# Kernel optimization log

Hardware: AMD Instinct MI355X
Metric: run time of the kernel (lower is better)

## Reference

```python
import jax, jax.numpy as jnp
import numpy as np

D = 768      # feature_dim
HD = 768     # hidden_dim
NH = 4       # num_heads
B, T1, T2 = 4, 128, 128
LN_EPS = 1e-5

def setup_inputs() -> dict:
    key = jax.random.key(0)
    ks = jax.random.split(key, 12)
    s = 0.02
    return {
        'speech_features': jax.random.normal(ks[0], (B, T1, D), jnp.float32),
        'phoneme_features': jax.random.normal(ks[1], (B, T2, D), jnp.float32),
        # per-head attention MLP: Linear(2D->HD), ReLU, Linear(HD->1); stacked over heads
        'W1': jax.random.normal(ks[2], (NH, 2 * D, HD), jnp.float32) * s,
        'b1': jnp.zeros((NH, HD), jnp.float32),
        'w2': jax.random.normal(ks[3], (NH, HD), jnp.float32) * s,
        'b2': jnp.zeros((NH,), jnp.float32),
        # fusion: Linear(2D->2HD), ReLU, Linear(2HD->D), LayerNorm(D)
        'Wf1': jax.random.normal(ks[4], (2 * D, 2 * HD), jnp.float32) * s,
        'bf1': jnp.zeros((2 * HD,), jnp.float32),
        'Wf2': jax.random.normal(ks[5], (2 * HD, D), jnp.float32) * s,
        'bf2': jnp.zeros((D,), jnp.float32),
        'ln_g': jnp.ones((D,), jnp.float32),
        'ln_b': jnp.zeros((D,), jnp.float32),
    }

def reference(speech_features, phoneme_features, W1, b1, w2, b2, Wf1, bf1, Wf2, bf2, ln_g, ln_b):
    d = speech_features.shape[-1]
    # Decompose Linear(cat([speech_t, phoneme])) = speech@W1[:d] + phoneme@W1[d:] + b1
    Wx, Wy = W1[:, :d, :], W1[:, d:, :]
    sx = jnp.einsum('btd,ndh->nbth', speech_features, Wx)   # [NH,B,T1,HD]
    py = jnp.einsum('bsd,ndh->nbsh', phoneme_features, Wy)  # [NH,B,T2,HD]
    hidden = jax.nn.relu(sx[:, :, :, None, :] + py[:, :, None, :, :]
                         + b1[:, None, None, None, :])      # [NH,B,T1,T2,HD]
    scores = jnp.einsum('nbtsh,nh->nbts', hidden, w2) + b2[:, None, None, None]
    attn = jax.nn.softmax(scores, axis=-1).mean(axis=0)     # [B,T1,T2]
    context = jnp.einsum('bts,bsd->btd', attn, phoneme_features)  # [B,T1,D]
    fused = jnp.concatenate([speech_features, context], axis=-1)  # [B,T1,2D]
    # dropout is identity in eval mode
    h = jax.nn.relu(fused @ Wf1 + bf1)
    out = h @ Wf2 + bf2
    mu = out.mean(axis=-1, keepdims=True)
    var = ((out - mu) ** 2).mean(axis=-1, keepdims=True)
    out = (out - mu) * jax.lax.rsqrt(var + LN_EPS) * ln_g + ln_b
    return out.mean(axis=1)  # [B,D]
```

## Files before the change

kernel.cpp:

```cpp
#include <hip/hip_runtime.h>
#include <cstddef>


#define D_  768
#define HD_ 768
#define NH_ 4
#define B_  4
#define T1_ 128
#define T2_ 128
#define M_  (B_*T1_)
#define LN_EPS_ 1e-5f

typedef unsigned short u16;
typedef unsigned int u32;
typedef _Float16 f16;
typedef _Float16 f16x2 __attribute__((ext_vector_type(2)));
typedef __bf16 bf16x8 __attribute__((ext_vector_type(8)));
typedef float f32x4 __attribute__((ext_vector_type(4)));

__device__ __forceinline__ u16 f2bf(float f) {
    union { float f; unsigned int u; } v; v.f = f;
    unsigned int u = v.u + (0x7FFFu + ((v.u >> 16) & 1u));
    return (u16)(u >> 16);
}
__device__ __forceinline__ u16 f16bits(f16 h) {
    return __builtin_bit_cast(unsigned short, h);
}
__device__ __forceinline__ f16x2 bcast2(u32 u) {
    return __builtin_bit_cast(f16x2, u);
}
__device__ __forceinline__ u32 splat2(u16 h) { return (u32)h * 0x10001u; }

template<bool RELU, int MODE>
__device__ __forceinline__ void gemm_mfma_body(
    const u16* __restrict__ A, int lda,
    const u16* __restrict__ Bt, int ldb,
    const float* __restrict__ bias,
    void* __restrict__ C, int ldc, int K, int m0, int n0)
{
    __shared__ __align__(16) u16 As[64][40];
    __shared__ __align__(16) u16 Bs[64][40];
    __shared__ u16 Ts[MODE == 3 ? 64 : 1][MODE == 3 ? 68 : 1];

    const int tid = threadIdx.x;
    const int row = tid >> 2;
    const int kq  = (tid & 3) << 3;
    const int lane = tid & 63;
    const int w  = tid >> 6;
    const int wr = (w >> 1) << 5;
    const int wc = (w & 1) << 5;
    const int l16 = lane & 15;
    const int lk8 = (lane >> 4) << 3;
    const int r4  = (lane >> 4) << 2;

    const u16* aptr = A + (size_t)(m0 + row) * lda + kq;
    const u16* bptr = Bt + (size_t)(n0 + row) * ldb + kq;

    f32x4 acc00 = {0.f,0.f,0.f,0.f}, acc01 = {0.f,0.f,0.f,0.f};
    f32x4 acc10 = {0.f,0.f,0.f,0.f}, acc11 = {0.f,0.f,0.f,0.f};

    uint4 a_nxt = *(const uint4*)aptr;
    uint4 b_nxt = *(const uint4*)bptr;

    for (int k0 = 0; k0 < K; k0 += 32) {
        __syncthreads();
        *(uint4*)&As[row][kq] = a_nxt;
        *(uint4*)&Bs[row][kq] = b_nxt;
        if (k0 + 32 < K) {
            a_nxt = *(const uint4*)(aptr + k0 + 32);
            b_nxt = *(const uint4*)(bptr + k0 + 32);
        }
        __syncthreads();
        bf16x8 af0 = *(const bf16x8*)&As[wr + l16][lk8];
        bf16x8 af1 = *(const bf16x8*)&As[wr + 16 + l16][lk8];
        bf16x8 bf0 = *(const bf16x8*)&Bs[wc + l16][lk8];
        bf16x8 bf1 = *(const bf16x8*)&Bs[wc + 16 + l16][lk8];
        acc00 = __builtin_amdgcn_mfma_f32_16x16x32_bf16(af0, bf0, acc00, 0, 0, 0);
        acc01 = __builtin_amdgcn_mfma_f32_16x16x32_bf16(af0, bf1, acc01, 0, 0, 0);
        acc10 = __builtin_amdgcn_mfma_f32_16x16x32_bf16(af1, bf0, acc10, 0, 0, 0);
        acc11 = __builtin_amdgcn_mfma_f32_16x16x32_bf16(af1, bf1, acc11, 0, 0, 0);
    }

#define EPI_FRAG(ACC, MF, NF)                                                  \
    {                                                                          \
        const int gcol = n0 + wc + (NF)*16 + l16;                              \
        const float bv = bias ? bias[gcol] : 0.f;                              \
        float v_[4];                                                           \
        _Pragma("unroll")                                                      \
        for (int r = 0; r < 4; r++) {                                          \
            float v = ACC[r] + bv;                                             \
            if (RELU) v = fmaxf(v, 0.f);                                       \
            v_[r] = v;                                                         \
        }                                                                      \
        const int lr0 = wr + (MF)*16 + r4;                                     \
        if (MODE == 3) {                                                       \
            const int lc = wc + (NF)*16 + l16;                                 \
            _Pragma("unroll")                                                  \
            for (int r = 0; r < 4; r++) Ts[lc][lr0 + r] = f16bits((f16)v_[r]); \
        } else {                                                               \
            _Pragma("unroll")                                                  \
            for (int r = 0; r < 4; r++) {                                      \
                const size_t off = (size_t)(m0 + lr0 + r) * ldc + gcol;        \
                if (MODE == 0) ((float*)C)[off] = v_[r];                       \
                else if (MODE == 1) ((u16*)C)[off] = f2bf(v_[r]);              \
                else ((u16*)C)[off] = f16bits((f16)v_[r]);                     \
            }                                                                  \
        }                                                                      \
    }
    EPI_FRAG(acc00, 0, 0) EPI_FRAG(acc01, 0, 1)
    EPI_FRAG(acc10, 1, 0) EPI_FRAG(acc11, 1, 1)
#undef EPI_FRAG

    if (MODE == 3) {
        __syncthreads();
        u16* cb = (u16*)C + (size_t)(m0 >> 7) * (768 * 128) + (m0 & 127);
#pragma unroll
        for (int u = 0; u < 4; u++) {
            const int i = tid + u * 256;
            const int hl = i >> 4;
            const int s4 = (i & 15) << 2;
            ushort4 o;
            o.x = Ts[hl][s4 + 0]; o.y = Ts[hl][s4 + 1];
            o.z = Ts[hl][s4 + 2]; o.w = Ts[hl][s4 + 3];
            *(ushort4*)(cb + (size_t)(n0 + hl) * 128 + s4) = o;
        }
    }
}

__global__ __launch_bounds__(256) void prep_kernel(
    const float* __restrict__ speech, const float* __restrict__ phon,
    const float* __restrict__ W1, const float* __restrict__ Wf1,
    const float* __restrict__ Wf2,
    u16* __restrict__ spb, u16* __restrict__ phb,
    u16* __restrict__ w1t, u16* __restrict__ wf1t, u16* __restrict__ wf2t)
{
    const int tid = threadIdx.x;
    int bid = blockIdx.x;
    if (bid < 768) {
        const bool isp = bid < 384;
        const float* in = isp ? speech : phon;
        u16* outb = isp ? spb : phb;
        const int i = ((isp ? bid : bid - 384) * 256 + tid) * 4;
        float4 v = *(const float4*)(in + i);
        ushort4 o;
        o.x = f2bf(v.x); o.y = f2bf(v.y); o.z = f2bf(v.z); o.w = f2bf(v.w);
        *(ushort4*)(outb + i) = o;
        return;
    }
    bid -= 768;
    const float* in; u16* outp; int tx, ty;
    if (bid < 4608) {
        const int z = bid / 1152, r = bid % 1152;
        tx = r % 24; ty = r / 24;
        in = W1 + (size_t)z * 1536 * 768; outp = w1t + (size_t)z * 768 * 1536;
    } else if (bid < 6912) {
        const int r = bid - 4608;
        tx = r % 48; ty = r / 48;
        in = Wf1; outp = wf1t;
    } else {
        const int r = bid - 6912;
        tx = r % 24; ty = r / 24;
        in = Wf2; outp = wf2t;
    }
    const int C = (bid >= 4608 && bid < 6912) ? 1536 : 768;
    const int c0 = tx * 32, r0 = ty * 32;
    __shared__ float tile[32][33];
    const int tr = tid >> 3, tc = (tid & 7) << 2;
    float4 v = *(const float4*)(in + (size_t)(r0 + tr) * C + c0 + tc);
    tile[tr][tc] = v.x; tile[tr][tc + 1] = v.y;
    tile[tr][tc + 2] = v.z; tile[tr][tc + 3] = v.w;
    __syncthreads();
    ushort4 o;
    o.x = f2bf(tile[tc + 0][tr]); o.y = f2bf(tile[tc + 1][tr]);
    o.z = f2bf(tile[tc + 2][tr]); o.w = f2bf(tile[tc + 3][tr]);
    *(ushort4*)(outp + (size_t)(c0 + tr) * 1536 + r0 + tc) = o;
}

__global__ __launch_bounds__(256) void gemm_sxpy_kernel(
    const u16* __restrict__ sp, const u16* __restrict__ ph,
    const u16* __restrict__ w1t, const float* __restrict__ b1,
    u16* __restrict__ sxf, u16* __restrict__ pyt)
{
    const int z = blockIdx.z;
    const int n = z & 3;
    const bool ispy = z >= 4;
    const u16* Bt = w1t + (size_t)n * 768 * 1536 + (ispy ? 768 : 0);
    if (!ispy) {
        gemm_mfma_body<false, 2>(sp, 768, Bt, 1536, b1 + n * HD_,
                                 sxf + (size_t)n * M_ * HD_, HD_, 768,
                                 blockIdx.y * 64, blockIdx.x * 64);
    } else {
        gemm_mfma_body<false, 3>(ph, 768, Bt, 1536, nullptr,
                                 pyt + (size_t)n * 4 * 768 * 128, 0, 768,
                                 blockIdx.y * 64, blockIdx.x * 64);
    }
}

template<bool RELU, int MODE>
__global__ __launch_bounds__(256) void gemm_mfma_kernel(
    const u16* __restrict__ A, int lda,
    const u16* __restrict__ Bt, int ldb,
    const float* __restrict__ bias,
    void* __restrict__ C, int ldc, int K)
{
    gemm_mfma_body<RELU, MODE>(A, lda, Bt, ldb, bias, C, ldc, K,
                               blockIdx.y * 64, blockIdx.x * 64);
}

__global__ __launch_bounds__(256) void scores_softmax_kernel(
    const u16* __restrict__ sxf,
    const u16* __restrict__ pyt,
    const float* __restrict__ w2,
    float* __restrict__ probs)
{
    const int bid = blockIdx.x;
    const int n = bid >> 7, b = (bid >> 5) & 3, t0 = (bid & 31) * 4;
    const int tid = threadIdx.x, lane = tid & 63, w = tid >> 6;

    __shared__ __align__(16) f16x2 sxs[4][768];
    __shared__ __align__(16) f16x2 w2s[768];

#pragma unroll
    for (int q = 0; q < 3; q++) {
        const int u = tid + q * 256;
        const int r = u / 192;
        const int h4 = (u % 192) * 4;
        ushort4 v = *(const ushort4*)(sxf + ((size_t)(n * 512 + b * 128 + t0 + r)) * 768 + h4);
        sxs[r][h4 + 0] = bcast2(splat2(v.x));
        sxs[r][h4 + 1] = bcast2(splat2(v.y));
        sxs[r][h4 + 2] = bcast2(splat2(v.z));
        sxs[r][h4 + 3] = bcast2(splat2(v.w));
    }
#pragma unroll
    for (int q = 0; q < 3; q++) {
        const int i = tid + q * 256;
        w2s[i] = bcast2(splat2(f16bits((f16)w2[n * 768 + i])));
    }
    __syncthreads();

    const f16x2* pypanel = (const f16x2*)(pyt + ((size_t)((n << 2) | b)) * 768 * 128) + lane;
    const f16x2 z2 = {(f16)0, (f16)0};

    float acc0 = 0.f, acc1 = 0.f;

    f16x2 b0[16], b1[16];
#pragma unroll
    for (int j = 0; j < 16; j++) b0[j] = pypanel[(size_t)j * 64];
#pragma unroll
    for (int j = 0; j < 16; j++) b1[j] = pypanel[(size_t)(16 + j) * 64];

    for (int hc = 0; hc < 768; hc += 32) {
        f16x2 a4[4] = {z2, z2, z2, z2};
#pragma unroll
        for (int j = 0; j < 16; j++) {
            f16x2 r_ = __builtin_elementwise_max(sxs[w][hc + j] + b0[j], z2);
            a4[j & 3] = __builtin_elementwise_fma(r_, w2s[hc + j], a4[j & 3]);
        }
        if (hc + 32 < 768) {
#pragma unroll
            for (int j = 0; j < 16; j++) b0[j] = pypanel[(size_t)(hc + 32 + j) * 64];
        }
#pragma unroll
        for (int j = 0; j < 16; j++) {
            f16x2 r_ = __builtin_elementwise_max(sxs[w][hc + 16 + j] + b1[j], z2);
            a4[j & 3] = __builtin_elementwise_fma(r_, w2s[hc + 16 + j], a4[j & 3]);
        }
        if (hc + 48 < 768) {
#pragma unroll
            for (int j = 0; j < 16; j++) b1[j] = pypanel[(size_t)(hc + 48 + j) * 64];
        }
#pragma unroll
        for (int k = 0; k < 4; k++) {
            acc0 += (float)a4[k].x;
            acc1 += (float)a4[k].y;
        }
    }

    float mx = fmaxf(acc0, acc1);
#pragma unroll
    for (int off = 32; off; off >>= 1) mx = fmaxf(mx, __shfl_xor(mx, off, 64));
    const float e0 = expf(acc0 - mx), e1 = expf(acc1 - mx);
    float sm = e0 + e1;
#pragma unroll
    for (int off = 32; off; off >>= 1) sm += __shfl_xor(sm, off, 64);
    const float inv = 0.25f / sm;
    float2 pr; pr.x = e0 * inv; pr.y = e1 * inv;
    *(float2*)&probs[((size_t)(n * 512 + b * 128 + t0 + w)) * 128 + 2 * lane] = pr;
}

__global__ __launch_bounds__(256) void context_fused_kernel(
    const float* __restrict__ probs, const float* __restrict__ phon,
    const float* __restrict__ speech, u16* __restrict__ fused)
{
    const int m = blockIdx.x;
    const int b = m >> 7;
    const int tid = threadIdx.x;
    __shared__ float attn[T2_];
    if (tid < T2_) {
        float a = 0.f;
#pragma unroll
        for (int n = 0; n < NH_; n++)
            a += probs[(size_t)(n * M_ + m) * T2_ + tid];
        attn[tid] = a;
    }
    __syncthreads();
    const float* ph = phon + (size_t)b * T2_ * D_;
#pragma unroll
    for (int j = 0; j < 3; j++) {
        const int d = tid + 256 * j;
        float acc = 0.f;
#pragma unroll 8
        for (int s = 0; s < T2_; s++)
            acc = fmaf(attn[s], ph[(size_t)s * D_ + d], acc);
        fused[(size_t)m * (2 * D_) + d] = f2bf(speech[(size_t)m * D_ + d]);
        fused[(size_t)m * (2 * D_) + D_ + d] = f2bf(acc);
    }
}

__global__ __launch_bounds__(256) void ln_fused_kernel(
    const float* __restrict__ x, const float* __restrict__ g,
    const float* __restrict__ lb, float* __restrict__ out)
{
    const int b = blockIdx.x, tid = threadIdx.x, lane = tid & 63, w = tid >> 6;
    __shared__ float rs[T1_];
    __shared__ float Sred[4];

    float prsum = 0.f;
    for (int i = 0; i < 32; i++) {
        const int row = w * 32 + i;
        const float4* x4 = (const float4*)(x + ((size_t)(b * T1_ + row)) * D_);
        float s = 0.f, ss = 0.f;
#pragma unroll
        for (int j = 0; j < 3; j++) {
            float4 v = x4[j * 64 + lane];
            s += v.x + v.y + v.z + v.w;
            ss += v.x * v.x + v.y * v.y + v.z * v.z + v.w * v.w;
        }
#pragma unroll
        for (int off = 32; off; off >>= 1) {
            s += __shfl_xor(s, off, 64);
            ss += __shfl_xor(ss, off, 64);
        }
        if (lane == 0) {
            const float mu = s * (1.f / D_);
            const float var = ss * (1.f / D_) - mu * mu;
            const float r = rsqrtf(var + LN_EPS_);
            rs[row] = r;
            prsum += mu * r;
        }
    }
    if (lane == 0) Sred[w] = prsum;
    __syncthreads();
    const float S = Sred[0] + Sred[1] + Sred[2] + Sred[3];
    const float* xb = x + (size_t)b * T1_ * D_;
#pragma unroll
    for (int j = 0; j < 3; j++) {
        const int d = tid + 256 * j;
        float acc = 0.f;
#pragma unroll 8
        for (int t = 0; t < T1_; t++)
            acc = fmaf(xb[(size_t)t * D_ + d], rs[t], acc);
        out[b * D_ + d] = g[d] * (acc - S) * (1.f / T1_) + lb[d];
    }
}

extern "C" void kernel_launch(void* const* d_in, const int* in_sizes, int n_in,
                              void* d_out, int out_size, void* d_ws, size_t ws_size,
                              hipStream_t stream)
{
    const float* speech = (const float*)d_in[0];
    const float* phon   = (const float*)d_in[1];
    const float* W1     = (const float*)d_in[2];
    const float* b1     = (const float*)d_in[3];
    const float* w2     = (const float*)d_in[4];
    const float* Wf1    = (const float*)d_in[6];
    const float* bf1    = (const float*)d_in[7];
    const float* Wf2    = (const float*)d_in[8];
    const float* bf2    = (const float*)d_in[9];
    const float* ln_g   = (const float*)d_in[10];
    const float* ln_b   = (const float*)d_in[11];
    float* out = (float*)d_out;

    char* w = (char*)d_ws;
    auto alloc = [&](size_t bytes) { char* p = w; w += (bytes + 1023) & ~(size_t)1023; return p; };
    u16* sp_bf  = (u16*)alloc((size_t)M_ * D_ * 2);
    u16* ph_bf  = (u16*)alloc((size_t)M_ * D_ * 2);
    u16* w1t    = (u16*)alloc((size_t)NH_ * 768 * 1536 * 2);
    u16* wf1t   = (u16*)alloc((size_t)1536 * 1536 * 2);
    u16* wf2t   = (u16*)alloc((size_t)768 * 1536 * 2);
    u16* sxf    = (u16*)alloc((size_t)NH_ * M_ * HD_ * 2);
    u16* pyt    = (u16*)alloc((size_t)NH_ * B_ * 768 * 128 * 2);
    float* probs  = (float*)alloc((size_t)NH_ * M_ * T2_ * 4);
    u16* fusedb = (u16*)alloc((size_t)M_ * 2 * D_ * 2);
    u16* hbuf   = (u16*)alloc((size_t)M_ * 2 * HD_ * 2);
    float* outpre = (float*)alloc((size_t)M_ * D_ * 4);

    hipLaunchKernelGGL(prep_kernel, dim3(8832), dim3(256), 0, stream,
                       speech, phon, W1, Wf1, Wf2, sp_bf, ph_bf, w1t, wf1t, wf2t);
    hipLaunchKernelGGL(gemm_sxpy_kernel, dim3(HD_ / 64, M_ / 64, 8), dim3(256), 0, stream,
                       sp_bf, ph_bf, w1t, b1, sxf, pyt);
    hipLaunchKernelGGL(scores_softmax_kernel, dim3(512), dim3(256), 0, stream,
                       sxf, pyt, w2, probs);
    hipLaunchKernelGGL(context_fused_kernel, dim3(M_), dim3(256), 0, stream,
                       probs, phon, speech, fusedb);
    hipLaunchKernelGGL((gemm_mfma_kernel<true, 1>), dim3(2 * HD_ / 64, M_ / 64), dim3(256), 0, stream,
                       fusedb, 2 * D_, wf1t, 1536, bf1, hbuf, 2 * HD_, 2 * D_);
    hipLaunchKernelGGL((gemm_mfma_kernel<false, 0>), dim3(D_ / 64, M_ / 64), dim3(256), 0, stream,
                       hbuf, 2 * HD_, wf2t, 1536, bf2, outpre, D_, 2 * HD_);
    hipLaunchKernelGGL(ln_fused_kernel, dim3(B_), dim3(256), 0, stream,
                       outpre, ln_g, ln_b, out);
}
```

Measured before the change: 134.8 us.

## Fuse scores with context, convert activations in GEMM loads, split LN blocks

Drops the separate activation-to-bf16 conversion pass. The sx/py GEMM now reads fp32 speech and phoneme data and packs it to bf16 while loading. The scores/softmax kernel now handles all four heads of one query row, one wave per head, and sums their probabilities in shared memory before computing the context row directly, which removes the probs buffer and one launch. The final LayerNorm-mean kernel is split across 12 blocks instead of 4 to expose more parallelism, at the cost of each block recomputing the row statistics.

New measurement: 127.8 us. 5.2% less time.

```diff
diff --git a/kernel.cpp b/kernel.cpp
--- a/kernel.cpp
+++ b/kernel.cpp
@@ -23,6 +23,9 @@
     unsigned int u = v.u + (0x7FFFu + ((v.u >> 16) & 1u));
     return (u16)(u >> 16);
 }
+__device__ __forceinline__ u32 pack_bf2(float lo, float hi) {
+    return (u32)f2bf(lo) | ((u32)f2bf(hi) << 16);
+}
 __device__ __forceinline__ u16 f16bits(f16 h) {
     return __builtin_bit_cast(unsigned short, h);
 }
@@ -31,9 +34,9 @@
 }
 __device__ __forceinline__ u32 splat2(u16 h) { return (u32)h * 0x10001u; }
 
-template<bool RELU, int MODE>
+template<bool RELU, int MODE, bool AF32>
 __device__ __forceinline__ void gemm_mfma_body(
-    const u16* __restrict__ A, int lda,
+    const void* __restrict__ Av, int lda,
     const u16* __restrict__ Bt, int ldb,
     const float* __restrict__ bias,
     void* __restrict__ C, int ldc, int K, int m0, int n0)
@@ -53,13 +56,26 @@
     const int lk8 = (lane >> 4) << 3;
     const int r4  = (lane >> 4) << 2;
 
-    const u16* aptr = A + (size_t)(m0 + row) * lda + kq;
-    const u16* bptr = Bt + (size_t)(n0 + row) * ldb + kq;
+    const u16*   aptr16 = (const u16*)Av + (size_t)(m0 + row) * lda + kq;
+    const float* aptrf  = (const float*)Av + (size_t)(m0 + row) * lda + kq;
+    const u16*   bptr   = Bt + (size_t)(n0 + row) * ldb + kq;
 
     f32x4 acc00 = {0.f,0.f,0.f,0.f}, acc01 = {0.f,0.f,0.f,0.f};
     f32x4 acc10 = {0.f,0.f,0.f,0.f}, acc11 = {0.f,0.f,0.f,0.f};
 
-    uint4 a_nxt = *(const uint4*)aptr;
+    auto loadA = [&](int k0) -> uint4 {
+        if (AF32) {
+            float4 ax = *(const float4*)(aptrf + k0);
+            float4 ay = *(const float4*)(aptrf + k0 + 4);
+            uint4 r;
+            r.x = pack_bf2(ax.x, ax.y); r.y = pack_bf2(ax.z, ax.w);
+            r.z = pack_bf2(ay.x, ay.y); r.w = pack_bf2(ay.z, ay.w);
+            return r;
+        }
+        return *(const uint4*)(aptr16 + k0);
+    };
+
+    uint4 a_nxt = loadA(0);
     uint4 b_nxt = *(const uint4*)bptr;
 
     for (int k0 = 0; k0 < K; k0 += 32) {
@@ -67,7 +83,7 @@
         *(uint4*)&As[row][kq] = a_nxt;
         *(uint4*)&Bs[row][kq] = b_nxt;
         if (k0 + 32 < K) {
-            a_nxt = *(const uint4*)(aptr + k0 + 32);
+            a_nxt = loadA(k0 + 32);
             b_nxt = *(const uint4*)(bptr + k0 + 32);
         }
         __syncthreads();
@@ -128,26 +144,12 @@
 }
 
 __global__ __launch_bounds__(256) void prep_kernel(
-    const float* __restrict__ speech, const float* __restrict__ phon,
     const float* __restrict__ W1, const float* __restrict__ Wf1,
     const float* __restrict__ Wf2,
-    u16* __restrict__ spb, u16* __restrict__ phb,
     u16* __restrict__ w1t, u16* __restrict__ wf1t, u16* __restrict__ wf2t)
 {
     const int tid = threadIdx.x;
     int bid = blockIdx.x;
-    if (bid < 768) {
-        const bool isp = bid < 384;
-        const float* in = isp ? speech : phon;
-        u16* outb = isp ? spb : phb;
-        const int i = ((isp ? bid : bid - 384) * 256 + tid) * 4;
-        float4 v = *(const float4*)(in + i);
-        ushort4 o;
-        o.x = f2bf(v.x); o.y = f2bf(v.y); o.z = f2bf(v.z); o.w = f2bf(v.w);
-        *(ushort4*)(outb + i) = o;
-        return;
-    }
-    bid -= 768;
     const float* in; u16* outp; int tx, ty;
     if (bid < 4608) {
         const int z = bid / 1152, r = bid % 1152;
@@ -177,7 +179,7 @@
 }
 
 __global__ __launch_bounds__(256) void gemm_sxpy_kernel(
-    const u16* __restrict__ sp, const u16* __restrict__ ph,
+    const float* __restrict__ sp, const float* __restrict__ ph,
     const u16* __restrict__ w1t, const float* __restrict__ b1,
     u16* __restrict__ sxf, u16* __restrict__ pyt)
 {
@@ -186,13 +188,13 @@
     const bool ispy = z >= 4;
     const u16* Bt = w1t + (size_t)n * 768 * 1536 + (ispy ? 768 : 0);
     if (!ispy) {
-        gemm_mfma_body<false, 2>(sp, 768, Bt, 1536, b1 + n * HD_,
-                                 sxf + (size_t)n * M_ * HD_, HD_, 768,
-                                 blockIdx.y * 64, blockIdx.x * 64);
+        gemm_mfma_body<false, 2, true>(sp, 768, Bt, 1536, b1 + n * HD_,
+                                       sxf + (size_t)n * M_ * HD_, HD_, 768,
+                                       blockIdx.y * 64, blockIdx.x * 64);
     } else {
-        gemm_mfma_body<false, 3>(ph, 768, Bt, 1536, nullptr,
-                                 pyt + (size_t)n * 4 * 768 * 128, 0, 768,
-                                 blockIdx.y * 64, blockIdx.x * 64);
+        gemm_mfma_body<false, 3, true>(ph, 768, Bt, 1536, nullptr,
+                                       pyt + (size_t)n * 4 * 768 * 128, 0, 768,
+                                       blockIdx.y * 64, blockIdx.x * 64);
     }
 }
 
@@ -203,42 +205,45 @@
     const float* __restrict__ bias,
     void* __restrict__ C, int ldc, int K)
 {
-    gemm_mfma_body<RELU, MODE>(A, lda, Bt, ldb, bias, C, ldc, K,
-                               blockIdx.y * 64, blockIdx.x * 64);
-}
-
-__global__ __launch_bounds__(256) void scores_softmax_kernel(
+    gemm_mfma_body<RELU, MODE, false>(A, lda, Bt, ldb, bias, C, ldc, K,
+                                      blockIdx.y * 64, blockIdx.x * 64);
+}
+
+__global__ __launch_bounds__(256) void scores_ctx_kernel(
     const u16* __restrict__ sxf,
     const u16* __restrict__ pyt,
     const float* __restrict__ w2,
-    float* __restrict__ probs)
+    const float* __restrict__ phon,
+    const float* __restrict__ speech,
+    u16* __restrict__ fused)
 {
     const int bid = blockIdx.x;
-    const int n = bid >> 7, b = (bid >> 5) & 3, t0 = (bid & 31) * 4;
+    const int b = bid >> 7, t = bid & 127;
+    const int m = b * 128 + t;
     const int tid = threadIdx.x, lane = tid & 63, w = tid >> 6;
 
     __shared__ __align__(16) f16x2 sxs[4][768];
-    __shared__ __align__(16) f16x2 w2s[768];
+    __shared__ __align__(16) f16x2 w2s[4][768];
+    __shared__ float attn4[4][128];
+    __shared__ float attn[128];
 
 #pragma unroll
     for (int q = 0; q < 3; q++) {
-        const int u = tid + q * 256;
-        const int r = u / 192;
-        const int h4 = (u % 192) * 4;
-        ushort4 v = *(const ushort4*)(sxf + ((size_t)(n * 512 + b * 128 + t0 + r)) * 768 + h4);
-        sxs[r][h4 + 0] = bcast2(splat2(v.x));
-        sxs[r][h4 + 1] = bcast2(splat2(v.y));
-        sxs[r][h4 + 2] = bcast2(splat2(v.z));
-        sxs[r][h4 + 3] = bcast2(splat2(v.w));
-    }
-#pragma unroll
-    for (int q = 0; q < 3; q++) {
-        const int i = tid + q * 256;
-        w2s[i] = bcast2(splat2(f16bits((f16)w2[n * 768 + i])));
-    }
-    __syncthreads();
-
-    const f16x2* pypanel = (const f16x2*)(pyt + ((size_t)((n << 2) | b)) * 768 * 128) + lane;
+        const int u = lane + 64 * q;
+        const int h4 = u * 4;
+        ushort4 v = *(const ushort4*)(sxf + ((size_t)(w * 512 + m)) * 768 + h4);
+        sxs[w][h4 + 0] = bcast2(splat2(v.x));
+        sxs[w][h4 + 1] = bcast2(splat2(v.y));
+        sxs[w][h4 + 2] = bcast2(splat2(v.z));
+        sxs[w][h4 + 3] = bcast2(splat2(v.w));
+        float4 wv = *(const float4*)(w2 + w * 768 + h4);
+        w2s[w][h4 + 0] = bcast2(splat2(f16bits((f16)wv.x)));
+        w2s[w][h4 + 1] = bcast2(splat2(f16bits((f16)wv.y)));
+        w2s[w][h4 + 2] = bcast2(splat2(f16bits((f16)wv.z)));
+        w2s[w][h4 + 3] = bcast2(splat2(f16bits((f16)wv.w)));
+    }
+
+    const f16x2* pypanel = (const f16x2*)(pyt + ((size_t)((w << 2) | b)) * 768 * 128) + lane;
     const f16x2 z2 = {(f16)0, (f16)0};
 
     float acc0 = 0.f, acc1 = 0.f;
@@ -254,7 +259,7 @@
 #pragma unroll
         for (int j = 0; j < 16; j++) {
             f16x2 r_ = __builtin_elementwise_max(sxs[w][hc + j] + b0[j], z2);
-            a4[j & 3] = __builtin_elementwise_fma(r_, w2s[hc + j], a4[j & 3]);
+            a4[j & 3] = __builtin_elementwise_fma(r_, w2s[w][hc + j], a4[j & 3]);
         }
         if (hc + 32 < 768) {
 #pragma unroll
@@ -263,7 +268,7 @@
 #pragma unroll
         for (int j = 0; j < 16; j++) {
             f16x2 r_ = __builtin_elementwise_max(sxs[w][hc + 16 + j] + b1[j], z2);
-            a4[j & 3] = __builtin_elementwise_fma(r_, w2s[hc + 16 + j], a4[j & 3]);
+            a4[j & 3] = __builtin_elementwise_fma(r_, w2s[w][hc + 16 + j], a4[j & 3]);
         }
         if (hc + 48 < 768) {
 #pragma unroll
@@ -285,35 +290,23 @@
     for (int off = 32; off; off >>= 1) sm += __shfl_xor(sm, off, 64);
     const float inv = 0.25f / sm;
     float2 pr; pr.x = e0 * inv; pr.y = e1 * inv;
-    *(float2*)&probs[((size_t)(n * 512 + b * 128 + t0 + w)) * 128 + 2 * lane] = pr;
-}
-
-__global__ __launch_bounds__(256) void context_fused_kernel(
-    const float* __restrict__ probs, const float* __restrict__ phon,
-    const float* __restrict__ speech, u16* __restrict__ fused)
-{
-    const int m = blockIdx.x;
-    const int b = m >> 7;
-    const int tid = threadIdx.x;
-    __shared__ float attn[T2_];
-    if (tid < T2_) {
-        float a = 0.f;
-#pragma unroll
-        for (int n = 0; n < NH_; n++)
-            a += probs[(size_t)(n * M_ + m) * T2_ + tid];
-        attn[tid] = a;
-    }
+    *(float2*)&attn4[w][2 * lane] = pr;
     __syncthreads();
-    const float* ph = phon + (size_t)b * T2_ * D_;
+
+    if (tid < 128)
+        attn[tid] = attn4[0][tid] + attn4[1][tid] + attn4[2][tid] + attn4[3][tid];
+    __syncthreads();
+
+    const float* ph = phon + (size_t)b * 128 * 768;
 #pragma unroll
     for (int j = 0; j < 3; j++) {
         const int d = tid + 256 * j;
         float acc = 0.f;
 #pragma unroll 8
-        for (int s = 0; s < T2_; s++)
-            acc = fmaf(attn[s], ph[(size_t)s * D_ + d], acc);
-        fused[(size_t)m * (2 * D_) + d] = f2bf(speech[(size_t)m * D_ + d]);
-        fused[(size_t)m * (2 * D_) + D_ + d] = f2bf(acc);
+        for (int s = 0; s < 128; s++)
+            acc = fmaf(attn[s], ph[(size_t)s * 768 + d], acc);
+        fused[(size_t)m * 1536 + d] = f2bf(speech[(size_t)m * 768 + d]);
+        fused[(size_t)m * 1536 + 768 + d] = f2bf(acc);
     }
 }
 
@@ -321,7 +314,8 @@
     const float* __restrict__ x, const float* __restrict__ g,
     const float* __restrict__ lb, float* __restrict__ out)
 {
-    const int b = blockIdx.x, tid = threadIdx.x, lane = tid & 63, w = tid >> 6;
+    const int b = blockIdx.x / 3, c = blockIdx.x % 3;
+    const int tid = threadIdx.x, lane = tid & 63, w = tid >> 6;
     __shared__ float rs[T1_];
     __shared__ float Sred[4];
 
@@ -353,15 +347,12 @@
     __syncthreads();
     const float S = Sred[0] + Sred[1] + Sred[2] + Sred[3];
     const float* xb = x + (size_t)b * T1_ * D_;
-#pragma unroll
-    for (int j = 0; j < 3; j++) {
-        const int d = tid + 256 * j;
-        float acc = 0.f;
+    const int d = c * 256 + tid;
+    float acc = 0.f;
 #pragma unroll 8
-        for (int t = 0; t < T1_; t++)
-            acc = fmaf(xb[(size_t)t * D_ + d], rs[t], acc);
-        out[b * D_ + d] = g[d] * (acc - S) * (1.f / T1_) + lb[d];
-    }
+    for (int t = 0; t < T1_; t++)
+        acc = fmaf(xb[(size_t)t * D_ + d], rs[t], acc);
+    out[b * D_ + d] = g[d] * (acc - S) * (1.f / T1_) + lb[d];
 }
 
 extern "C" void kernel_launch(void* const* d_in, const int* in_sizes, int n_in,
@@ -383,30 +374,25 @@
 
     char* w = (char*)d_ws;
     auto alloc = [&](size_t bytes) { char* p = w; w += (bytes + 1023) & ~(size_t)1023; return p; };
-    u16* sp_bf  = (u16*)alloc((size_t)M_ * D_ * 2);
-    u16* ph_bf  = (u16*)alloc((size_t)M_ * D_ * 2);
     u16* w1t    = (u16*)alloc((size_t)NH_ * 768 * 1536 * 2);
     u16* wf1t   = (u16*)alloc((size_t)1536 * 1536 * 2);
     u16* wf2t   = (u16*)alloc((size_t)768 * 1536 * 2);
     u16* sxf    = (u16*)alloc((size_t)NH_ * M_ * HD_ * 2);
     u16* pyt    = (u16*)alloc((size_t)NH_ * B_ * 768 * 128 * 2);
-    float* probs  = (float*)alloc((size_t)NH_ * M_ * T2_ * 4);
     u16* fusedb = (u16*)alloc((size_t)M_ * 2 * D_ * 2);
     u16* hbuf   = (u16*)alloc((size_t)M_ * 2 * HD_ * 2);
     float* outpre = (float*)alloc((size_t)M_ * D_ * 4);
 
-    hipLaunchKernelGGL(prep_kernel, dim3(8832), dim3(256), 0, stream,
-                       speech, phon, W1, Wf1, Wf2, sp_bf, ph_bf, w1t, wf1t, wf2t);
+    hipLaunchKernelGGL(prep_kernel, dim3(8064), dim3(256), 0, stream,
+                       W1, Wf1, Wf2, w1t, wf1t, wf2t);
     hipLaunchKernelGGL(gemm_sxpy_kernel, dim3(HD_ / 64, M_ / 64, 8), dim3(256), 0, stream,
-                       sp_bf, ph_bf, w1t, b1, sxf, pyt);
-    hipLaunchKernelGGL(scores_softmax_kernel, dim3(512), dim3(256), 0, stream,
-                       sxf, pyt, w2, probs);
-    hipLaunchKernelGGL(context_fused_kernel, dim3(M_), dim3(256), 0, stream,
-                       probs, phon, speech, fusedb);
+                       speech, phon, w1t, b1, sxf, pyt);
+    hipLaunchKernelGGL(scores_ctx_kernel, dim3(512), dim3(256), 0, stream,
+                       sxf, pyt, w2, phon, speech, fusedb);
     hipLaunchKernelGGL((gemm_mfma_kernel<true, 1>), dim3(2 * HD_ / 64, M_ / 64), dim3(256), 0, stream,
                        fusedb, 2 * D_, wf1t, 1536, bf1, hbuf, 2 * HD_, 2 * D_);
     hipLaunchKernelGGL((gemm_mfma_kernel<false, 0>), dim3(D_ / 64, M_ / 64), dim3(256), 0, stream,
                        hbuf, 2 * HD_, wf2t, 1536, bf2, outpre, D_, 2 * HD_);
-    hipLaunchKernelGGL(ln_fused_kernel, dim3(B_), dim3(256), 0, stream,
+    hipLaunchKernelGGL(ln_fused_kernel, dim3(12), dim3(256), 0, stream,
                        outpre, ln_g, ln_b, out);
 }
```
